# Kernel tuning notes

Hardware: AMD Instinct MI355X
Metric: run time of the kernel (lower is better)

## Reference

```python
import jax, jax.numpy as jnp
import numpy as np

EMB = 2048
H = 16
Q_RANK = 1536
KV_RANK = 512
ROPE_D = 64
NOPE_D = 64
V_D = 128
QK_D = ROPE_D + NOPE_D  # 128
ROPE_BASE = 10000.0
SCALING = 1.0  # query_pre_attn_scalar ** -0.5 with scalar=1.0


def apply_rope(x):
    """torchtune-style interleaved RoPE. x: (B, S, H, D)."""
    S, D = x.shape[1], x.shape[-1]
    theta = 1.0 / (ROPE_BASE ** (jnp.arange(0, D, 2, dtype=jnp.float32) / D))  # (D/2,)
    ang = jnp.arange(S, dtype=jnp.float32)[:, None] * theta[None, :]  # (S, D/2)
    cos = jnp.cos(ang)[None, :, None, :]
    sin = jnp.sin(ang)[None, :, None, :]
    xf = x.astype(jnp.float32).reshape(*x.shape[:-1], D // 2, 2)
    x0, x1 = xf[..., 0], xf[..., 1]
    out = jnp.stack([x0 * cos - x1 * sin, x1 * cos + x0 * sin], axis=-1)
    return out.reshape(x.shape).astype(x.dtype)


def setup_inputs() -> dict:
    key = jax.random.key(0)
    ks = jax.random.split(key, 6)
    s = lambda fan_in: 1.0 / np.sqrt(fan_in)
    return {
        "x": jax.random.normal(ks[0], (2, 2048, EMB), dtype=jnp.float32),
        "q_a_w": jax.random.uniform(ks[1], (Q_RANK, EMB), jnp.float32, -s(EMB), s(EMB)),
        "q_b_w": jax.random.uniform(ks[2], (H * QK_D, Q_RANK), jnp.float32, -s(Q_RANK), s(Q_RANK)),
        "kv_a_w": jax.random.uniform(ks[3], (KV_RANK + ROPE_D, EMB), jnp.float32, -s(EMB), s(EMB)),
        "kv_b_w": jax.random.uniform(ks[4], (H * (NOPE_D + V_D), KV_RANK), jnp.float32, -s(KV_RANK), s(KV_RANK)),
        "o_w": jax.random.uniform(ks[5], (EMB, H * V_D), jnp.float32, -s(H * V_D), s(H * V_D)),
    }


def reference(x, q_a_w, q_b_w, kv_a_w, kv_b_w, o_w):
    B, S, _ = x.shape
    # LoRA-compressed Q projection
    q = (x @ q_a_w.T) @ q_b_w.T  # (B, S, H*QK_D)
    q = q.reshape(B, S, H, QK_D).transpose(0, 2, 1, 3)  # (B, H, S, QK_D)
    q_pass, q_rot = q[..., :NOPE_D], q[..., NOPE_D:]
    # Compressed KV with shared rope key
    ckv = x @ kv_a_w.T  # (B, S, KV_RANK + ROPE_D)
    k_pass_c, k_rot = ckv[..., :KV_RANK], ckv[..., KV_RANK:]
    kvb = (k_pass_c @ kv_b_w.T).reshape(B, S, H, NOPE_D + V_D).transpose(0, 2, 1, 3)
    k_pass, v = kvb[..., :NOPE_D], kvb[..., NOPE_D:]  # (B,H,S,NOPE_D), (B,H,S,V_D)
    # RoPE (applied in (B,S,H,D) layout, as in the original)
    q_rot = apply_rope(q_rot.transpose(0, 2, 1, 3)).transpose(0, 2, 1, 3)
    k_rot = apply_rope(k_rot[:, :, None, :])  # (B, S, 1, ROPE_D), shared across heads
    k_rot = jnp.broadcast_to(k_rot.transpose(0, 2, 1, 3), (B, H, S, ROPE_D))
    query = jnp.concatenate([q_pass, q_rot], axis=-1)  # (B, H, S, QK_D)
    key = jnp.concatenate([k_pass, k_rot], axis=-1)
    # NOTE: original passes attention_mask=None -> no causal mask applied.
    scores = jnp.einsum("bhqd,bhkd->bhqk", query, key) * SCALING
    attn = jax.nn.softmax(scores.astype(jnp.float32), axis=-1).astype(query.dtype)
    out = jnp.einsum("bhqk,bhkd->bhqd", attn, v)  # (B, H, S, V_D)
    out = out.transpose(0, 2, 1, 3).reshape(B, S, H * V_D)
    return out @ o_w.T
```

## Files before the change

### kernel.cpp

```cpp
#include <hip/hip_runtime.h>
#include <stdint.h>

#define EMB 2048
#define NH 16
#define QRANK 1536
#define KVRANK 512
#define ROPED 64
#define NOPED 64
#define VD 128
#define QKD 128
#define SEQ 2048
#define BATCH 2
#define BS 4096
#define BHD 32
#define NCOMB 2112
#define LOG2E 1.4426950408889634f
#define NT (SEQ / 64)

typedef __attribute__((ext_vector_type(4))) float f32x4;
typedef __attribute__((ext_vector_type(8))) short s16x8;
typedef __attribute__((ext_vector_type(4))) short s16x4;
typedef __attribute__((ext_vector_type(2))) unsigned int u32x2;

__device__ __forceinline__ float bf2f(unsigned short u) {
  return __uint_as_float(((unsigned int)u) << 16);
}
__device__ __forceinline__ unsigned short f2bf(float f) {
  unsigned int u = __float_as_uint(f);
  u += 0x7fff + ((u >> 16) & 1);
  return (unsigned short)(u >> 16);
}

__device__ __forceinline__ float vexp2(float x) {
#if __has_builtin(__builtin_amdgcn_exp2f)
  return __builtin_amdgcn_exp2f(x);
#else
  return exp2f(x);
#endif
}

__device__ __forceinline__ unsigned int pk_bf16_trunc(float e0, float e1) {
#if __has_builtin(__builtin_amdgcn_perm)
  return __builtin_amdgcn_perm(__float_as_uint(e1), __float_as_uint(e0), 0x07060302u);
#else
  return (__float_as_uint(e1) & 0xffff0000u) | (__float_as_uint(e0) >> 16);
#endif
}

__device__ __forceinline__ void pl32swap(unsigned int& a, unsigned int& b) {
#if __has_builtin(__builtin_amdgcn_permlane32_swap)
  u32x2 r = __builtin_amdgcn_permlane32_swap(a, b, false, false);
  a = r.x; b = r.y;
#else
  asm("v_permlane32_swap_b32 %0, %1" : "+v"(a), "+v"(b));
#endif
}
__device__ __forceinline__ void pl16swap(unsigned int& a, unsigned int& b) {
#if __has_builtin(__builtin_amdgcn_permlane16_swap)
  u32x2 r = __builtin_amdgcn_permlane16_swap(a, b, false, false);
  a = r.x; b = r.y;
#else
  asm("v_permlane16_swap_b32 %0, %1" : "+v"(a), "+v"(b));
#endif
}

__device__ __forceinline__ void gld_lds16(const unsigned short* g, unsigned short* l) {
  __builtin_amdgcn_global_load_lds((const __attribute__((address_space(1))) void*)g,
                                   (__attribute__((address_space(3))) void*)l,
                                   16, 0, 0);
}

#define N4_X   (BS * EMB / 4)
#define N4_QA  (QRANK * EMB / 4)
#define N4_KVA ((KVRANK + ROPED) * EMB / 4)
#define N4_QB  (NH * QKD * QRANK / 4)
#define N4_KVB (NH * 192 * KVRANK / 4)
#define N4_O   (EMB * NH * VD / 4)
#define N4_TOT (N4_X + N4_QA + N4_KVA + N4_QB + N4_KVB + N4_O)

__global__ void cast_all(const float* __restrict__ x, const float* __restrict__ qa,
                         const float* __restrict__ kva, const float* __restrict__ qb,
                         const float* __restrict__ kvb, const float* __restrict__ ow,
                         unsigned short* __restrict__ Xb, unsigned short* __restrict__ Wcomb,
                         unsigned short* __restrict__ Wqb, unsigned short* __restrict__ Wkvb,
                         unsigned short* __restrict__ Wo) {
  int i = blockIdx.x * blockDim.x + threadIdx.x;
  int stride = gridDim.x * blockDim.x;
  for (; i < N4_TOT; i += stride) {
    const float4* src;
    ushort4* dst;
    int j = i;
    if (j < N4_X) { src = (const float4*)x; dst = (ushort4*)Xb; }
    else if ((j -= N4_X) < N4_QA) { src = (const float4*)qa; dst = (ushort4*)Wcomb; }
    else if ((j -= N4_QA) < N4_KVA) { src = (const float4*)kva; dst = (ushort4*)(Wcomb + (size_t)QRANK * EMB); }
    else if ((j -= N4_KVA) < N4_QB) { src = (const float4*)qb; dst = (ushort4*)Wqb; }
    else if ((j -= N4_QB) < N4_KVB) { src = (const float4*)kvb; dst = (ushort4*)Wkvb; }
    else { j -= N4_KVB; src = (const float4*)ow; dst = (ushort4*)Wo; }
    float4 v = src[j];
    ushort4 o;
    o.x = f2bf(v.x); o.y = f2bf(v.y); o.z = f2bf(v.z); o.w = f2bf(v.w);
    dst[j] = o;
  }
}

template <int OUT_F32>
__global__ __launch_bounds__(256, 2) void gemm_bt(
    const unsigned short* __restrict__ A, int lda,
    const unsigned short* __restrict__ W, int ldw,
    void* __restrict__ C, int M, int N, int K)
{
  __shared__ __align__(16) unsigned short As[128 * 64];
  __shared__ __align__(16) unsigned short Ws[128 * 64];
  const int tid = threadIdx.x;
  const int wave = tid >> 6;
  const int lane = tid & 63;
  const int ln = lane & 15;
  const int quad = lane >> 4;
  const int bm = blockIdx.y * 128;
  const int bn = blockIdx.x * 128;
  const int wm = (wave >> 1) * 64;
  const int wn = (wave & 1) * 64;

  f32x4 acc[4][4] = {};

  const int rel8 = lane >> 3;
  const int csw = ((lane & 7) ^ rel8) * 8;

  for (int k0 = 0; k0 < K; k0 += 64) {
#pragma unroll
    for (int it = 0; it < 4; ++it) {
      int rb = wave * 32 + it * 8;
      gld_lds16(A + (size_t)(bm + rb + rel8) * lda + k0 + csw, &As[rb * 64]);
    }
#pragma unroll
    for (int it = 0; it < 4; ++it) {
      int rb = wave * 32 + it * 8;
      int wr = bn + rb + rel8;
      if (wr >= N) wr = N - 1;
      gld_lds16(W + (size_t)wr * ldw + k0 + csw, &Ws[rb * 64]);
    }
    __syncthreads();
#pragma unroll
    for (int kk = 0; kk < 64; kk += 32) {
      s16x8 a[4], b[4];
#pragma unroll
      for (int mt = 0; mt < 4; ++mt)
        a[mt] = *(const s16x8*)&As[(wm + mt * 16 + ln) * 64 + ((kk / 8 + quad) ^ (ln & 7)) * 8];
#pragma unroll
      for (int nt = 0; nt < 4; ++nt)
        b[nt] = *(const s16x8*)&Ws[(wn + nt * 16 + ln) * 64 + ((kk / 8 + quad) ^ (ln & 7)) * 8];
#pragma unroll
      for (int mt = 0; mt < 4; ++mt)
#pragma unroll
        for (int nt = 0; nt < 4; ++nt)
          acc[mt][nt] = __builtin_amdgcn_mfma_f32_16x16x32_bf16(a[mt], b[nt], acc[mt][nt], 0, 0, 0);
    }
    __syncthreads();
  }
#pragma unroll
  for (int mt = 0; mt < 4; ++mt) {
    int row = bm + wm + mt * 16 + quad * 4;
#pragma unroll
    for (int nt = 0; nt < 4; ++nt) {
      int col = bn + wn + nt * 16 + ln;
      if (col < N) {
#pragma unroll
        for (int r = 0; r < 4; ++r) {
          float v = acc[mt][nt][r];
          if (OUT_F32)
            ((float*)C)[(size_t)(row + r) * N + col] = v;
          else
            ((unsigned short*)C)[(size_t)(row + r) * N + col] = f2bf(v);
        }
      }
    }
  }
}

__global__ __launch_bounds__(256, 2) void gemm_q_rope(
    const unsigned short* __restrict__ A, int lda,
    const unsigned short* __restrict__ W, int ldw,
    unsigned short* __restrict__ Qry, int K)
{
  __shared__ __align__(16) unsigned short As[128 * 64];
  __shared__ __align__(16) unsigned short Ws[128 * 64];
  const int tid = threadIdx.x;
  const int wave = tid >> 6;
  const int lane = tid & 63;
  const int ln = lane & 15;
  const int quad = lane >> 4;
  const int bm = blockIdx.y * 128;
  const int bn = blockIdx.x * 128;
  const int wm = (wave >> 1) * 64;
  const int wn = (wave & 1) * 64;

  f32x4 acc[4][4] = {};
  const int rel8 = lane >> 3;
  const int csw = ((lane & 7) ^ rel8) * 8;

  for (int k0 = 0; k0 < K; k0 += 64) {
#pragma unroll
    for (int it = 0; it < 4; ++it) {
      int rb = wave * 32 + it * 8;
      gld_lds16(A + (size_t)(bm + rb + rel8) * lda + k0 + csw, &As[rb * 64]);
    }
#pragma unroll
    for (int it = 0; it < 4; ++it) {
      int rb = wave * 32 + it * 8;
      gld_lds16(W + (size_t)(bn + rb + rel8) * ldw + k0 + csw, &Ws[rb * 64]);
    }
    __syncthreads();
#pragma unroll
    for (int kk = 0; kk < 64; kk += 32) {
      s16x8 a[4], b[4];
#pragma unroll
      for (int mt = 0; mt < 4; ++mt)
        a[mt] = *(const s16x8*)&As[(wm + mt * 16 + ln) * 64 + ((kk / 8 + quad) ^ (ln & 7)) * 8];
#pragma unroll
      for (int nt = 0; nt < 4; ++nt)
        b[nt] = *(const s16x8*)&Ws[(wn + nt * 16 + ln) * 64 + ((kk / 8 + quad) ^ (ln & 7)) * 8];
#pragma unroll
      for (int mt = 0; mt < 4; ++mt)
#pragma unroll
        for (int nt = 0; nt < 4; ++nt)
          acc[mt][nt] = __builtin_amdgcn_mfma_f32_16x16x32_bf16(a[mt], b[nt], acc[mt][nt], 0, 0, 0);
    }
    __syncthreads();
  }
  const bool odd = (ln & 1);
#pragma unroll
  for (int mt = 0; mt < 4; ++mt) {
    int rowb = bm + wm + mt * 16 + quad * 4;
#pragma unroll
    for (int nt = 0; nt < 4; ++nt) {
      int col = bn + wn + nt * 16 + ln;
      int h = col >> 7, d = col & 127;
#pragma unroll
      for (int r = 0; r < 4; ++r) {
        float v = acc[mt][nt][r];
        float other = __shfl_xor(v, 1);
        int row = rowb + r;
        int b = row >> 11, s = row & 2047;
        float y = v;
        if (d >= NOPED) {
          int i = (d - NOPED) >> 1;
          float theta = exp2f(-(float)i * (13.287712379549449f / 32.f));
          float ang = (float)s * theta;
          float sn, c;
          sincosf(ang, &sn, &c);
          y = v * c + (odd ? other * sn : -other * sn);
        }
        y *= LOG2E;
        Qry[((size_t)(b * NH + h) * SEQ + s) * QKD + d] = f2bf(y);
      }
    }
  }
}

__global__ void prep_key(const unsigned short* __restrict__ kvb,
                         const unsigned short* __restrict__ cqkv,
                         unsigned short* __restrict__ Key) {
  __shared__ unsigned short krot[ROPED];
  int bs = blockIdx.x;
  int b = bs >> 11, s = bs & 2047;
  int tid = threadIdx.x;
  if (tid < 32) {
    int i = tid;
    float x0 = bf2f(cqkv[(size_t)bs * NCOMB + QRANK + KVRANK + 2 * i]);
    float x1 = bf2f(cqkv[(size_t)bs * NCOMB + QRANK + KVRANK + 2 * i + 1]);
    float theta = exp2f(-(float)i * (13.287712379549449f / 32.f));
    float ang = (float)s * theta;
    float sn, c;
    sincosf(ang, &sn, &c);
    krot[2 * i] = f2bf(x0 * c - x1 * sn);
    krot[2 * i + 1] = f2bf(x1 * c + x0 * sn);
  }
  __syncthreads();
  for (int idx = tid; idx < NH * QKD; idx += 256) {
    int h = idx >> 7, d = idx & 127;
    unsigned short v;
    if (d < NOPED)
      v = kvb[(size_t)bs * (NH * 192) + h * 192 + d];
    else
      v = krot[d - NOPED];
    Key[((size_t)(b * NH + h) * SEQ + s) * QKD + d] = v;
  }
}

__global__ void transpose_v(const unsigned short* __restrict__ kvb, unsigned short* __restrict__ VT) {
  __shared__ unsigned short tile[64][132];
  int blk = blockIdx.x;
  int bh = blk >> 5, st = blk & 31;
  int b = bh >> 4, h = bh & 15;
  int s0 = st * 64;
  int tid = threadIdx.x;
  for (int idx = tid; idx < 64 * 128; idx += 256) {
    int sl = idx >> 7, d = idx & 127;
    tile[sl][d] = kvb[((size_t)(b * SEQ + s0 + sl)) * (NH * 192) + h * 192 + NOPED + d];
  }
  __syncthreads();
  for (int idx = tid; idx < 64 * 128; idx += 256) {
    int d = idx >> 6, sl = idx & 63;
    VT[((size_t)bh * VD + d) * SEQ + s0 + sl] = tile[sl][d];
  }
}

__global__ __launch_bounds__(256, 2) void flash_attn(
    const unsigned short* __restrict__ Q,
    const unsigned short* __restrict__ Kt,
    const unsigned short* __restrict__ VT,
    unsigned short* __restrict__ O)
{
  __shared__ __align__(16) unsigned short Ks[2][64 * 128];
  __shared__ __align__(16) unsigned short Vs[3][128 * 64];

  const int tid = threadIdx.x;
  const int wave = tid >> 6;
  const int lane = tid & 63;
  const int ln = lane & 15;
  const int quad = lane >> 4;
  const int bh = blockIdx.x;
  const int q0 = blockIdx.y * 128;
  const int b = bh >> 4, h = bh & 15;

  s16x8 qa[2][4];
#pragma unroll
  for (int mt = 0; mt < 2; ++mt) {
    const unsigned short* qrow = Q + ((size_t)bh * SEQ + q0 + wave * 32 + mt * 16 + ln) * QKD;
#pragma unroll
    for (int kx = 0; kx < 4; ++kx)
      qa[mt][kx] = *(const s16x8*)(qrow + kx * 32 + quad * 8);
  }

  const int krel = lane >> 4, kcch = lane & 15;
  const int vrel8 = lane >> 3;
  const int vc8 = (lane & 7) ^ vrel8;

  auto stage = [&](unsigned short* Kd, unsigned short* Vd, int kt) {
#pragma unroll
    for (int it = 0; it < 4; ++it) {
      int rb = wave * 16 + it * 4;
      int rr = rb + krel;
      int c = kcch ^ (rr & 15);
      gld_lds16(Kt + ((size_t)bh * SEQ + kt * 64 + rr) * QKD + c * 8, Kd + rb * 128);
    }
#pragma unroll
    for (int it = 0; it < 4; ++it) {
      int rb = wave * 32 + it * 8;
      gld_lds16(VT + ((size_t)bh * VD + rb + vrel8) * SEQ + kt * 64 + vc8 * 8, Vd + rb * 64);
    }
  };

  f32x4 o[2][8] = {};
  float l_i[2] = {0.f, 0.f};

  auto sc_init = [&](f32x4 (&sc)[2][4]) {
#pragma unroll
    for (int mt = 0; mt < 2; ++mt)
#pragma unroll
      for (int t = 0; t < 4; ++t)
        sc[mt][t] = (f32x4){-20.f, -20.f, -20.f, -20.f};
  };
  auto qk_kx = [&](int kx, const unsigned short* Kc, f32x4 (&sc)[2][4]) {
    s16x8 ak[4];
#pragma unroll
    for (int t = 0; t < 4; ++t)
      ak[t] = *(const s16x8*)&Kc[(t * 16 + ln) * 128 + ((kx * 4 + quad) ^ ln) * 8];
#pragma unroll
    for (int mt = 0; mt < 2; ++mt)
#pragma unroll
      for (int t = 0; t < 4; ++t)
        sc[mt][t] = __builtin_amdgcn_mfma_f32_16x16x32_bf16(ak[t], qa[mt][kx], sc[mt][t], 0, 0, 0);
  };
  auto sm_mt = [&](int mt, f32x4 (&sc)[2][4], s16x8 (&pfrag)[2][2]) {
    float rs = 0.f;
    unsigned int pw[4][2];
#pragma unroll
    for (int t = 0; t < 4; ++t) {
      float e0 = vexp2(sc[mt][t][0]);
      float e1 = vexp2(sc[mt][t][1]);
      float e2 = vexp2(sc[mt][t][2]);
      float e3 = vexp2(sc[mt][t][3]);
      unsigned int p01 = pk_bf16_trunc(e0, e1);
      unsigned int p23 = pk_bf16_trunc(e2, e3);
      pw[t][0] = p01; pw[t][1] = p23;
      rs += (__uint_as_float(p01 << 16) + __uint_as_float(p01 & 0xffff0000u))
          + (__uint_as_float(p23 << 16) + __uint_as_float(p23 & 0xffff0000u));
    }
    rs += __shfl_xor(rs, 16);
    rs += __shfl_xor(rs, 32);
    l_i[mt] += rs;
#pragma unroll
    for (int W = 0; W < 2; ++W) {
      unsigned int u0 = pw[2 * W][0], v0 = pw[2 * W + 1][0];
      unsigned int u1 = pw[2 * W][1], v1 = pw[2 * W + 1][1];
      pl32swap(u0, v0); pl16swap(u0, v0);
      pl32swap(u1, v1); pl16swap(u1, v1);
      union { unsigned int u[4]; s16x8 v; } fb;
      fb.u[0] = u0;
      fb.u[1] = u1;
      fb.u[2] = v0;
      fb.u[3] = v1;
      pfrag[mt][W] = fb.v;
    }
  };
  auto pv_half = [&](int half, const unsigned short* Vc, s16x8 (&pfrag)[2][2]) {
#pragma unroll
    for (int dd = 0; dd < 4; ++dd) {
      int dt = half * 4 + dd;
      s16x8 av0 = *(const s16x8*)&Vc[(dt * 16 + ln) * 64 + ((quad ^ (ln & 7)) * 8)];
      s16x8 av1 = *(const s16x8*)&Vc[(dt * 16 + ln) * 64 + (((4 + quad) ^ (ln & 7)) * 8)];
#pragma unroll
      for (int mt = 0; mt < 2; ++mt) {
        o[mt][dt] = __builtin_amdgcn_mfma_f32_16x16x32_bf16(av0, pfrag[mt][0], o[mt][dt], 0, 0, 0);
        o[mt][dt] = __builtin_amdgcn_mfma_f32_16x16x32_bf16(av1, pfrag[mt][1], o[mt][dt], 0, 0, 0);
      }
    }
  };

  auto iter = [&](int kt, f32x4 (&scP)[2][4], f32x4 (&scC)[2][4]) {
    asm volatile("s_waitcnt vmcnt(0)" ::: "memory");
    asm volatile("s_barrier" ::: "memory");
    if (kt + 1 < NT)
      stage(Ks[(kt + 1) & 1], Vs[(kt + 1) % 3], kt + 1);
    const unsigned short* Kc = Ks[kt & 1];
    const unsigned short* Vp = Vs[(kt - 1) % 3];
    s16x8 pfrag[2][2];
    __builtin_amdgcn_s_setprio(1);
    sc_init(scC);
    qk_kx(0, Kc, scC);
    sm_mt(0, scP, pfrag);
    qk_kx(1, Kc, scC);
    sm_mt(1, scP, pfrag);
    qk_kx(2, Kc, scC);
    pv_half(0, Vp, pfrag);
    qk_kx(3, Kc, scC);
    pv_half(1, Vp, pfrag);
    __builtin_amdgcn_s_setprio(0);
  };

  f32x4 scA[2][4], scB[2][4];

  stage(Ks[0], Vs[0], 0);
  asm volatile("s_waitcnt vmcnt(0)" ::: "memory");
  asm volatile("s_barrier" ::: "memory");
  stage(Ks[1], Vs[1], 1);
  __builtin_amdgcn_s_setprio(1);
  sc_init(scA);
  qk_kx(0, Ks[0], scA);
  qk_kx(1, Ks[0], scA);
  qk_kx(2, Ks[0], scA);
  qk_kx(3, Ks[0], scA);
  __builtin_amdgcn_s_setprio(0);

  int kt = 1;
#pragma unroll 1
  for (int p = 0; p < 15; ++p, kt += 2) {
    iter(kt, scA, scB);
    iter(kt + 1, scB, scA);
  }
  iter(31, scA, scB);

  {
    s16x8 pfrag[2][2];
    sm_mt(0, scB, pfrag);
    sm_mt(1, scB, pfrag);
    pv_half(0, Vs[1], pfrag);
    pv_half(1, Vs[1], pfrag);
  }

#pragma unroll
  for (int mt = 0; mt < 2; ++mt) {
    float inv = 1.f / l_i[mt];
    int s = q0 + wave * 32 + mt * 16 + ln;
    size_t rowbase = ((size_t)b * SEQ + s) * (NH * VD) + h * VD;
#pragma unroll
    for (int dt = 0; dt < 8; ++dt) {
      ushort4 pk;
      pk.x = f2bf(o[mt][dt][0] * inv);
      pk.y = f2bf(o[mt][dt][1] * inv);
      pk.z = f2bf(o[mt][dt][2] * inv);
      pk.w = f2bf(o[mt][dt][3] * inv);
      *(ushort4*)&O[rowbase + dt * 16 + quad * 4] = pk;
    }
  }
}

extern "C" void kernel_launch(void* const* d_in, const int* in_sizes, int n_in,
                              void* d_out, int out_size, void* d_ws, size_t ws_size,
                              hipStream_t stream) {
  const float* x_f    = (const float*)d_in[0];
  const float* qaw_f  = (const float*)d_in[1];
  const float* qbw_f  = (const float*)d_in[2];
  const float* kvaw_f = (const float*)d_in[3];
  const float* kvbw_f = (const float*)d_in[4];
  const float* ow_f   = (const float*)d_in[5];

  char* ws = (char*)d_ws;
  size_t off = 0;
  auto alloc = [&](size_t n) {
    unsigned short* p = (unsigned short*)(ws + off);
    off = (off + n * 2 + 255) & ~(size_t)255;
    return p;
  };
  unsigned short* Xb    = alloc((size_t)BS * EMB);
  unsigned short* Wcomb = alloc((size_t)NCOMB * EMB);
  unsigned short* Wqb   = alloc((size_t)(NH * QKD) * QRANK);
  unsigned short* Wkvb  = alloc((size_t)(NH * 192) * KVRANK);
  unsigned short* Wo    = alloc((size_t)EMB * (NH * VD));
  unsigned short* CQKV  = alloc((size_t)BS * NCOMB);
  unsigned short* KVB   = alloc((size_t)BS * (NH * 192));
  unsigned short* Qry   = alloc((size_t)BHD * SEQ * QKD);
  unsigned short* Key   = alloc((size_t)BHD * SEQ * QKD);
  unsigned short* Vt    = alloc((size_t)BHD * VD * SEQ);
  unsigned short* AO    = alloc((size_t)BS * (NH * VD));

  cast_all<<<dim3(8192), 256, 0, stream>>>(x_f, qaw_f, kvaw_f, qbw_f, kvbw_f, ow_f,
                                           Xb, Wcomb, Wqb, Wkvb, Wo);

  gemm_bt<0><<<dim3((NCOMB + 127) / 128, BS / 128), 256, 0, stream>>>(
      Xb, EMB, Wcomb, EMB, CQKV, BS, NCOMB, EMB);
  gemm_q_rope<<<dim3((NH * QKD) / 128, BS / 128), 256, 0, stream>>>(
      CQKV, NCOMB, Wqb, QRANK, Qry, QRANK);
  gemm_bt<0><<<dim3((NH * 192) / 128, BS / 128), 256, 0, stream>>>(
      CQKV + QRANK, NCOMB, Wkvb, KVRANK, KVB, BS, NH * 192, KVRANK);

  prep_key<<<dim3(BS), 256, 0, stream>>>(KVB, CQKV, Key);
  transpose_v<<<dim3(BHD * (SEQ / 64)), 256, 0, stream>>>(KVB, Vt);

  flash_attn<<<dim3(BHD, SEQ / 128), 256, 0, stream>>>(Qry, Key, Vt, AO);

  gemm_bt<1><<<dim3(EMB / 128, BS / 128), 256, 0, stream>>>(
      AO, NH * VD, Wo, NH * VD, d_out, BS, EMB, NH * VD);
}
```

Before: 386.5 us.

## Double-buffer GEMM LDS tiles and fuse key prep with V transpose

Both GEMM kernels now keep two LDS buffers for A and W. The next K-tile is prefetched with direct-to-LDS loads while MFMAs run on the current one, using explicit vmcnt waits and barriers in place of two __syncthreads per iteration. The separate prep_key and transpose_v kernels are merged into one prep_kv kernel, which removes a launch and vectorizes the V loads. In exchange, LDS use per GEMM block doubles to 64KB, which may limit occupancy, and the merged kernel recomputes the key RoPE once per head.

New measurement: 387.4 us. Within noise of the previous version (+0.2%).

```diff
diff --git a/kernel.cpp b/kernel.cpp
--- a/kernel.cpp
+++ b/kernel.cpp
@@ -109,8 +109,8 @@
     const unsigned short* __restrict__ W, int ldw,
     void* __restrict__ C, int M, int N, int K)
 {
-  __shared__ __align__(16) unsigned short As[128 * 64];
-  __shared__ __align__(16) unsigned short Ws[128 * 64];
+  __shared__ __align__(16) unsigned short As[2][128 * 64];
+  __shared__ __align__(16) unsigned short Ws[2][128 * 64];
   const int tid = threadIdx.x;
   const int wave = tid >> 6;
   const int lane = tid & 63;
@@ -126,36 +126,49 @@
   const int rel8 = lane >> 3;
   const int csw = ((lane & 7) ^ rel8) * 8;
 
-  for (int k0 = 0; k0 < K; k0 += 64) {
+  auto stage = [&](int buf, int k0) {
 #pragma unroll
     for (int it = 0; it < 4; ++it) {
       int rb = wave * 32 + it * 8;
-      gld_lds16(A + (size_t)(bm + rb + rel8) * lda + k0 + csw, &As[rb * 64]);
+      gld_lds16(A + (size_t)(bm + rb + rel8) * lda + k0 + csw, &As[buf][rb * 64]);
     }
 #pragma unroll
     for (int it = 0; it < 4; ++it) {
       int rb = wave * 32 + it * 8;
       int wr = bn + rb + rel8;
       if (wr >= N) wr = N - 1;
-      gld_lds16(W + (size_t)wr * ldw + k0 + csw, &Ws[rb * 64]);
-    }
-    __syncthreads();
+      gld_lds16(W + (size_t)wr * ldw + k0 + csw, &Ws[buf][rb * 64]);
+    }
+  };
+
+  const int KT = K >> 6;
+  stage(0, 0);
+  for (int t = 0; t < KT; ++t) {
+    if (t + 1 < KT) {
+      stage((t + 1) & 1, (t + 1) << 6);
+      asm volatile("s_waitcnt vmcnt(8)" ::: "memory");
+    } else {
+      asm volatile("s_waitcnt vmcnt(0)" ::: "memory");
+    }
+    asm volatile("s_barrier" ::: "memory");
+    const unsigned short* Ac = As[t & 1];
+    const unsigned short* Wc = Ws[t & 1];
 #pragma unroll
     for (int kk = 0; kk < 64; kk += 32) {
       s16x8 a[4], b[4];
 #pragma unroll
       for (int mt = 0; mt < 4; ++mt)
-        a[mt] = *(const s16x8*)&As[(wm + mt * 16 + ln) * 64 + ((kk / 8 + quad) ^ (ln & 7)) * 8];
+        a[mt] = *(const s16x8*)&Ac[(wm + mt * 16 + ln) * 64 + ((kk / 8 + quad) ^ (ln & 7)) * 8];
 #pragma unroll
       for (int nt = 0; nt < 4; ++nt)
-        b[nt] = *(const s16x8*)&Ws[(wn + nt * 16 + ln) * 64 + ((kk / 8 + quad) ^ (ln & 7)) * 8];
+        b[nt] = *(const s16x8*)&Wc[(wn + nt * 16 + ln) * 64 + ((kk / 8 + quad) ^ (ln & 7)) * 8];
 #pragma unroll
       for (int mt = 0; mt < 4; ++mt)
 #pragma unroll
         for (int nt = 0; nt < 4; ++nt)
           acc[mt][nt] = __builtin_amdgcn_mfma_f32_16x16x32_bf16(a[mt], b[nt], acc[mt][nt], 0, 0, 0);
     }
-    __syncthreads();
+    asm volatile("s_barrier" ::: "memory");
   }
 #pragma unroll
   for (int mt = 0; mt < 4; ++mt) {
@@ -182,8 +195,8 @@
     const unsigned short* __restrict__ W, int ldw,
     unsigned short* __restrict__ Qry, int K)
 {
-  __shared__ __align__(16) unsigned short As[128 * 64];
-  __shared__ __align__(16) unsigned short Ws[128 * 64];
+  __shared__ __align__(16) unsigned short As[2][128 * 64];
+  __shared__ __align__(16) unsigned short Ws[2][128 * 64];
   const int tid = threadIdx.x;
   const int wave = tid >> 6;
   const int lane = tid & 63;
@@ -198,34 +211,47 @@
   const int rel8 = lane >> 3;
   const int csw = ((lane & 7) ^ rel8) * 8;
 
-  for (int k0 = 0; k0 < K; k0 += 64) {
+  auto stage = [&](int buf, int k0) {
 #pragma unroll
     for (int it = 0; it < 4; ++it) {
       int rb = wave * 32 + it * 8;
-      gld_lds16(A + (size_t)(bm + rb + rel8) * lda + k0 + csw, &As[rb * 64]);
+      gld_lds16(A + (size_t)(bm + rb + rel8) * lda + k0 + csw, &As[buf][rb * 64]);
     }
 #pragma unroll
     for (int it = 0; it < 4; ++it) {
       int rb = wave * 32 + it * 8;
-      gld_lds16(W + (size_t)(bn + rb + rel8) * ldw + k0 + csw, &Ws[rb * 64]);
-    }
-    __syncthreads();
+      gld_lds16(W + (size_t)(bn + rb + rel8) * ldw + k0 + csw, &Ws[buf][rb * 64]);
+    }
+  };
+
+  const int KT = K >> 6;
+  stage(0, 0);
+  for (int t = 0; t < KT; ++t) {
+    if (t + 1 < KT) {
+      stage((t + 1) & 1, (t + 1) << 6);
+      asm volatile("s_waitcnt vmcnt(8)" ::: "memory");
+    } else {
+      asm volatile("s_waitcnt vmcnt(0)" ::: "memory");
+    }
+    asm volatile("s_barrier" ::: "memory");
+    const unsigned short* Ac = As[t & 1];
+    const unsigned short* Wc = Ws[t & 1];
 #pragma unroll
     for (int kk = 0; kk < 64; kk += 32) {
       s16x8 a[4], b[4];
 #pragma unroll
       for (int mt = 0; mt < 4; ++mt)
-        a[mt] = *(const s16x8*)&As[(wm + mt * 16 + ln) * 64 + ((kk / 8 + quad) ^ (ln & 7)) * 8];
+        a[mt] = *(const s16x8*)&Ac[(wm + mt * 16 + ln) * 64 + ((kk / 8 + quad) ^ (ln & 7)) * 8];
 #pragma unroll
       for (int nt = 0; nt < 4; ++nt)
-        b[nt] = *(const s16x8*)&Ws[(wn + nt * 16 + ln) * 64 + ((kk / 8 + quad) ^ (ln & 7)) * 8];
+        b[nt] = *(const s16x8*)&Wc[(wn + nt * 16 + ln) * 64 + ((kk / 8 + quad) ^ (ln & 7)) * 8];
 #pragma unroll
       for (int mt = 0; mt < 4; ++mt)
 #pragma unroll
         for (int nt = 0; nt < 4; ++nt)
           acc[mt][nt] = __builtin_amdgcn_mfma_f32_16x16x32_bf16(a[mt], b[nt], acc[mt][nt], 0, 0, 0);
     }
-    __syncthreads();
+    asm volatile("s_barrier" ::: "memory");
   }
   const bool odd = (ln & 1);
 #pragma unroll
@@ -257,51 +283,49 @@
   }
 }
 
-__global__ void prep_key(const unsigned short* __restrict__ kvb,
-                         const unsigned short* __restrict__ cqkv,
-                         unsigned short* __restrict__ Key) {
-  __shared__ unsigned short krot[ROPED];
-  int bs = blockIdx.x;
-  int b = bs >> 11, s = bs & 2047;
-  int tid = threadIdx.x;
-  if (tid < 32) {
-    int i = tid;
-    float x0 = bf2f(cqkv[(size_t)bs * NCOMB + QRANK + KVRANK + 2 * i]);
-    float x1 = bf2f(cqkv[(size_t)bs * NCOMB + QRANK + KVRANK + 2 * i + 1]);
-    float theta = exp2f(-(float)i * (13.287712379549449f / 32.f));
-    float ang = (float)s * theta;
-    float sn, c;
-    sincosf(ang, &sn, &c);
-    krot[2 * i] = f2bf(x0 * c - x1 * sn);
-    krot[2 * i + 1] = f2bf(x1 * c + x0 * sn);
-  }
-  __syncthreads();
-  for (int idx = tid; idx < NH * QKD; idx += 256) {
-    int h = idx >> 7, d = idx & 127;
-    unsigned short v;
-    if (d < NOPED)
-      v = kvb[(size_t)bs * (NH * 192) + h * 192 + d];
-    else
-      v = krot[d - NOPED];
-    Key[((size_t)(b * NH + h) * SEQ + s) * QKD + d] = v;
-  }
-}
-
-__global__ void transpose_v(const unsigned short* __restrict__ kvb, unsigned short* __restrict__ VT) {
-  __shared__ unsigned short tile[64][132];
+__global__ void prep_kv(const unsigned short* __restrict__ kvb,
+                        const unsigned short* __restrict__ cqkv,
+                        unsigned short* __restrict__ Key,
+                        unsigned short* __restrict__ VT) {
+  __shared__ unsigned short vt[64][132];
+  __shared__ unsigned short kr[64][64];
   int blk = blockIdx.x;
   int bh = blk >> 5, st = blk & 31;
   int b = bh >> 4, h = bh & 15;
   int s0 = st * 64;
   int tid = threadIdx.x;
+
+  for (int idx = tid; idx < 64 * 32; idx += 256) {
+    int sl = idx >> 5, i = idx & 31;
+    int s = s0 + sl;
+    const unsigned short* rp = cqkv + (size_t)(b * SEQ + s) * NCOMB + QRANK + KVRANK;
+    float x0 = bf2f(rp[2 * i]);
+    float x1 = bf2f(rp[2 * i + 1]);
+    float theta = exp2f(-(float)i * (13.287712379549449f / 32.f));
+    float ang = (float)s * theta;
+    float sn, c;
+    sincosf(ang, &sn, &c);
+    kr[sl][2 * i] = f2bf(x0 * c - x1 * sn);
+    kr[sl][2 * i + 1] = f2bf(x1 * c + x0 * sn);
+  }
+  for (int idx = tid; idx < 64 * 16; idx += 256) {
+    int sl = idx >> 4, dc = idx & 15;
+    s16x8 v = *(const s16x8*)(kvb + (size_t)(b * SEQ + s0 + sl) * (NH * 192) + h * 192 + NOPED + dc * 8);
+    *(s16x8*)&vt[sl][dc * 8] = v;
+  }
+  __syncthreads();
   for (int idx = tid; idx < 64 * 128; idx += 256) {
     int sl = idx >> 7, d = idx & 127;
-    tile[sl][d] = kvb[((size_t)(b * SEQ + s0 + sl)) * (NH * 192) + h * 192 + NOPED + d];
-  }
-  __syncthreads();
+    unsigned short v;
+    if (d < NOPED)
+      v = kvb[(size_t)(b * SEQ + s0 + sl) * (NH * 192) + h * 192 + d];
+    else
+      v = kr[sl][d - NOPED];
+    Key[((size_t)bh * SEQ + s0 + sl) * QKD + d] = v;
+  }
   for (int idx = tid; idx < 64 * 128; idx += 256) {
     int d = idx >> 6, sl = idx & 63;
-    VT[((size_t)bh * VD + d) * SEQ + s0 + sl] = tile[sl][d];
+    VT[((size_t)bh * VD + d) * SEQ + s0 + sl] = vt[sl][d];
   }
 }
 
@@ -525,8 +549,7 @@
   gemm_bt<0><<<dim3((NH * 192) / 128, BS / 128), 256, 0, stream>>>(
       CQKV + QRANK, NCOMB, Wkvb, KVRANK, KVB, BS, NH * 192, KVRANK);
 
-  prep_key<<<dim3(BS), 256, 0, stream>>>(KVB, CQKV, Key);
-  transpose_v<<<dim3(BHD * (SEQ / 64)), 256, 0, stream>>>(KVB, Vt);
+  prep_kv<<<dim3(BHD * (SEQ / 64)), 256, 0, stream>>>(KVB, CQKV, Key, Vt);
 
   flash_attn<<<dim3(BHD, SEQ / 128), 256, 0, stream>>>(Qry, Key, Vt, AO);
 
```

## Fuse key prep with V transpose and double flash-attention block to 512 threads

Applied to the files above, without the earlier changes.

Merges the key-building kernel and the V transpose into one per-(head, 64-row tile) kernel that applies RoPE to a tile of rope keys in shared memory and writes both Key and transposed V. This removes one launch and reads the kvb data in tile order with vectorized V loads. Flash attention now runs 8 waves per block over 256 queries, so each staged K/V tile is shared by twice as many query rows and each wave issues half the staging loads. The larger blocks cut the grid in half and may reduce occupancy. The code depends on unseen wave-indexed addressing scaling correctly to 8 waves.

Measured after the change: 374.8 us. 1.03x faster.

```diff
diff --git a/kernel.cpp b/kernel.cpp
--- a/kernel.cpp
+++ b/kernel.cpp
@@ -257,55 +257,53 @@
   }
 }
 
-__global__ void prep_key(const unsigned short* __restrict__ kvb,
-                         const unsigned short* __restrict__ cqkv,
-                         unsigned short* __restrict__ Key) {
-  __shared__ unsigned short krot[ROPED];
-  int bs = blockIdx.x;
-  int b = bs >> 11, s = bs & 2047;
-  int tid = threadIdx.x;
-  if (tid < 32) {
-    int i = tid;
-    float x0 = bf2f(cqkv[(size_t)bs * NCOMB + QRANK + KVRANK + 2 * i]);
-    float x1 = bf2f(cqkv[(size_t)bs * NCOMB + QRANK + KVRANK + 2 * i + 1]);
-    float theta = exp2f(-(float)i * (13.287712379549449f / 32.f));
-    float ang = (float)s * theta;
-    float sn, c;
-    sincosf(ang, &sn, &c);
-    krot[2 * i] = f2bf(x0 * c - x1 * sn);
-    krot[2 * i + 1] = f2bf(x1 * c + x0 * sn);
-  }
-  __syncthreads();
-  for (int idx = tid; idx < NH * QKD; idx += 256) {
-    int h = idx >> 7, d = idx & 127;
-    unsigned short v;
-    if (d < NOPED)
-      v = kvb[(size_t)bs * (NH * 192) + h * 192 + d];
-    else
-      v = krot[d - NOPED];
-    Key[((size_t)(b * NH + h) * SEQ + s) * QKD + d] = v;
-  }
-}
-
-__global__ void transpose_v(const unsigned short* __restrict__ kvb, unsigned short* __restrict__ VT) {
-  __shared__ unsigned short tile[64][132];
+__global__ void prep_kv(const unsigned short* __restrict__ kvb,
+                        const unsigned short* __restrict__ cqkv,
+                        unsigned short* __restrict__ Key,
+                        unsigned short* __restrict__ VT) {
+  __shared__ unsigned short vt[64][132];
+  __shared__ unsigned short kr[64][64];
   int blk = blockIdx.x;
   int bh = blk >> 5, st = blk & 31;
   int b = bh >> 4, h = bh & 15;
   int s0 = st * 64;
   int tid = threadIdx.x;
+
+  for (int idx = tid; idx < 64 * 32; idx += 256) {
+    int sl = idx >> 5, i = idx & 31;
+    int s = s0 + sl;
+    const unsigned short* rp = cqkv + (size_t)(b * SEQ + s) * NCOMB + QRANK + KVRANK;
+    float x0 = bf2f(rp[2 * i]);
+    float x1 = bf2f(rp[2 * i + 1]);
+    float theta = exp2f(-(float)i * (13.287712379549449f / 32.f));
+    float ang = (float)s * theta;
+    float sn, c;
+    sincosf(ang, &sn, &c);
+    kr[sl][2 * i] = f2bf(x0 * c - x1 * sn);
+    kr[sl][2 * i + 1] = f2bf(x1 * c + x0 * sn);
+  }
+  for (int idx = tid; idx < 64 * 16; idx += 256) {
+    int sl = idx >> 4, dc = idx & 15;
+    s16x8 v = *(const s16x8*)(kvb + (size_t)(b * SEQ + s0 + sl) * (NH * 192) + h * 192 + NOPED + dc * 8);
+    *(s16x8*)&vt[sl][dc * 8] = v;
+  }
+  __syncthreads();
   for (int idx = tid; idx < 64 * 128; idx += 256) {
     int sl = idx >> 7, d = idx & 127;
-    tile[sl][d] = kvb[((size_t)(b * SEQ + s0 + sl)) * (NH * 192) + h * 192 + NOPED + d];
-  }
-  __syncthreads();
+    unsigned short v;
+    if (d < NOPED)
+      v = kvb[(size_t)(b * SEQ + s0 + sl) * (NH * 192) + h * 192 + d];
+    else
+      v = kr[sl][d - NOPED];
+    Key[((size_t)bh * SEQ + s0 + sl) * QKD + d] = v;
+  }
   for (int idx = tid; idx < 64 * 128; idx += 256) {
     int d = idx >> 6, sl = idx & 63;
-    VT[((size_t)bh * VD + d) * SEQ + s0 + sl] = tile[sl][d];
-  }
-}
-
-__global__ __launch_bounds__(256, 2) void flash_attn(
+    VT[((size_t)bh * VD + d) * SEQ + s0 + sl] = vt[sl][d];
+  }
+}
+
+__global__ __launch_bounds__(512, 2) void flash_attn(
     const unsigned short* __restrict__ Q,
     const unsigned short* __restrict__ Kt,
     const unsigned short* __restrict__ VT,
@@ -320,7 +318,7 @@
   const int ln = lane & 15;
   const int quad = lane >> 4;
   const int bh = blockIdx.x;
-  const int q0 = blockIdx.y * 128;
+  const int q0 = blockIdx.y * 256;
   const int b = bh >> 4, h = bh & 15;
 
   s16x8 qa[2][4];
@@ -338,15 +336,15 @@
 
   auto stage = [&](unsigned short* Kd, unsigned short* Vd, int kt) {
 #pragma unroll
-    for (int it = 0; it < 4; ++it) {
-      int rb = wave * 16 + it * 4;
+    for (int it = 0; it < 2; ++it) {
+      int rb = wave * 8 + it * 4;
       int rr = rb + krel;
       int c = kcch ^ (rr & 15);
       gld_lds16(Kt + ((size_t)bh * SEQ + kt * 64 + rr) * QKD + c * 8, Kd + rb * 128);
     }
 #pragma unroll
-    for (int it = 0; it < 4; ++it) {
-      int rb = wave * 32 + it * 8;
+    for (int it = 0; it < 2; ++it) {
+      int rb = wave * 16 + it * 8;
       gld_lds16(VT + ((size_t)bh * VD + rb + vrel8) * SEQ + kt * 64 + vc8 * 8, Vd + rb * 64);
     }
   };
@@ -525,10 +523,9 @@
   gemm_bt<0><<<dim3((NH * 192) / 128, BS / 128), 256, 0, stream>>>(
       CQKV + QRANK, NCOMB, Wkvb, KVRANK, KVB, BS, NH * 192, KVRANK);
 
-  prep_key<<<dim3(BS), 256, 0, stream>>>(KVB, CQKV, Key);
-  transpose_v<<<dim3(BHD * (SEQ / 64)), 256, 0, stream>>>(KVB, Vt);
-
-  flash_attn<<<dim3(BHD, SEQ / 128), 256, 0, stream>>>(Qry, Key, Vt, AO);
+  prep_kv<<<dim3(BHD * (SEQ / 64)), 256, 0, stream>>>(KVB, CQKV, Key, Vt);
+
+  flash_attn<<<dim3(BHD, SEQ / 256), 512, 0, stream>>>(Qry, Key, Vt, AO);
 
   gemm_bt<1><<<dim3(EMB / 128, BS / 128), 256, 0, stream>>>(
       AO, NH * VD, Wo, NH * VD, d_out, BS, EMB, NH * VD);
```
